# Kernel optimization log

Hardware: AMD Instinct MI355X
Metric: run time of the kernel (lower is better)

The kernel has to match this reference:

```python
import jax, jax.numpy as jnp
import numpy as np

NEG_INF = -1e9


def setup_inputs() -> dict:
    key = jax.random.key(0)
    ks = jax.random.split(key, 8)
    B, S, D = 8, 2048, 1024
    scale = 1.0 / np.sqrt(D)
    src = jax.random.normal(ks[0], (B, S, D), dtype=jnp.float32)
    pad_len = jax.random.randint(ks[1], (B,), 0, S // 10)
    pos = jnp.arange(S)[None, :]
    src_padding_mask = jnp.where(pos >= (S - pad_len)[:, None], NEG_INF, 0.0).astype(jnp.float32)[:, :, None]
    # causal (subsequent) additive mask [S,S]
    src_subsq_mask = jnp.where(jnp.triu(jnp.ones((S, S), dtype=bool), k=1), NEG_INF, 0.0).astype(jnp.float32)
    Wk = jax.random.normal(ks[2], (D, D), dtype=jnp.float32) * scale
    Wv = jax.random.normal(ks[3], (D, D), dtype=jnp.float32) * scale
    Wq = jax.random.normal(ks[4], (D, D), dtype=jnp.float32) * scale
    bk = jnp.zeros((D,), dtype=jnp.float32)
    bv = jnp.zeros((D,), dtype=jnp.float32)
    bq = jnp.zeros((D,), dtype=jnp.float32)
    return {"src": src, "src_padding_mask": src_padding_mask, "src_subsq_mask": src_subsq_mask,
            "Wk": Wk, "bk": bk, "Wv": Wv, "bv": bv, "Wq": Wq, "bq": bq}


def reference(src, src_padding_mask, src_subsq_mask, Wk, bk, Wv, bv, Wq, bq):
    d_model = src.shape[-1]
    # torch nn.Linear: x @ W.T + b
    keys = jnp.einsum('bsd,ed->bse', src, Wk) + bk
    values = jnp.einsum('bsd,ed->bse', src, Wv) + bv
    queries = jnp.einsum('bsd,ed->bse', src, Wq) + bq
    sqrt_d = jnp.asarray(d_model, src.dtype) ** 0.5
    att = jnp.einsum('bqd,bkd->bqk', queries, keys) / sqrt_d   # [B,S,S]
    att = att + jnp.swapaxes(src_padding_mask, 1, 2)           # [B,1,S] broadcast
    att = att + src_subsq_mask[None, :, :]                      # [1,S,S] broadcast
    att_softmax = jax.nn.softmax(att, axis=2)
    att_out = jnp.einsum('bqk,bkd->bqd', att_softmax, values)
    return att_out
```

## Files before the change

### kernel.cpp

```cpp
#include <hip/hip_runtime.h>
#include <cstdint>
#include <cstddef>

#define BATCH 8
#define SEQ   2048
#define DM    1024

typedef _Float16 half8 __attribute__((ext_vector_type(8)));
typedef _Float16 half4v __attribute__((ext_vector_type(4)));
typedef float floatx4 __attribute__((ext_vector_type(4)));
typedef float float4v __attribute__((ext_vector_type(4)));

#define GLOBAL_AS __attribute__((address_space(1)))
#define LDS_AS    __attribute__((address_space(3)))

__device__ __forceinline__ void gl_lds16(const _Float16* g, _Float16* l) {
    __builtin_amdgcn_global_load_lds((const GLOBAL_AS void*)g, (LDS_AS void*)l, 16, 0, 0);
}

__device__ __forceinline__ void stage128(const _Float16* __restrict__ g, int ld, int k0,
                                         _Float16* l, int wave, int lane) {
    const int rw = wave * 8 + (lane >> 3);
    const int sl = lane & 7;
    #pragma unroll
    for (int i = 0; i < 2; i++) {
        const int r = i * 64 + rw;
        gl_lds16(g + (size_t)r * ld + k0 + ((sl ^ (r & 7)) << 3),
                 l + ((i * 64 + wave * 8) << 6));
    }
}

#define SCHED __builtin_amdgcn_sched_barrier(0)
#define BAR   __builtin_amdgcn_s_barrier()
#define WAIT_VM0    asm volatile("s_waitcnt vmcnt(0)" ::: "memory")
#define WAIT_LGKM12 asm volatile("s_waitcnt lgkmcnt(12)" ::: "memory")
#define WAIT_LGKM0  asm volatile("s_waitcnt lgkmcnt(0)" ::: "memory")

#define RD_SET(AV, BV, BUF, SL)                                               \
    _Pragma("unroll")                                                         \
    for (int i_ = 0; i_ < 4; i_++)                                            \
        AV[i_] = *(const half8*)&SA[BUF][aoff + i_ * 1024 + (SL)];            \
    _Pragma("unroll")                                                         \
    for (int i_ = 0; i_ < 4; i_++)                                            \
        AV[4 + i_] = *(const half8*)&SA[BUF][aoff + 8192 + i_ * 1024 + (SL)]; \
    _Pragma("unroll")                                                         \
    for (int j_ = 0; j_ < 2; j_++)                                            \
        BV[j_] = *(const half8*)&SB[BUF][boff + j_ * 4096 + (SL)];            \
    _Pragma("unroll")                                                         \
    for (int j_ = 0; j_ < 2; j_++)                                            \
        BV[2 + j_] = *(const half8*)&SB[BUF][boff + 8192 + j_ * 4096 + (SL)];

#define MM_SET(AV, BV)                                                        \
    __builtin_amdgcn_s_setprio(1);                                            \
    _Pragma("unroll")                                                         \
    for (int i_ = 0; i_ < 8; i_++)                                            \
        _Pragma("unroll")                                                     \
        for (int j_ = 0; j_ < 4; j_++)                                        \
            acc[i_][j_] = __builtin_amdgcn_mfma_f32_16x16x32_f16(             \
                AV[i_], BV[j_], acc[i_][j_], 0, 0, 0);                        \
    __builtin_amdgcn_s_setprio(0);

__device__ __forceinline__ void gemm256_rr(
    const _Float16* __restrict__ A, const _Float16* __restrict__ B,
    int lda, int ldb, int nkt,
    _Float16 (&SA)[2][16384], _Float16 (&SB)[2][16384],
    floatx4 (&acc)[8][4])
{
    const int t = threadIdx.x;
    const int wave = t >> 6, lane = t & 63;
    const int l15 = lane & 15, kq = lane >> 4;
    const int wm = wave >> 2, wn = wave & 3;

    const int aoff = (wm * 64 + l15) << 6;
    const int boff = (wn * 16 + l15) << 6;
    const int sl0 = ((kq ^ (l15 & 7)) << 3);
    const int sl1 = (((4 + kq) ^ (l15 & 7)) << 3);

    const _Float16* A128 = A + (size_t)128 * lda;
    const _Float16* B128 = B + (size_t)128 * ldb;

    half8 a0[8], b0[4], a1[8], b1[4];

    stage128(A,    lda, 0, &SA[0][0],    wave, lane);
    stage128(A128, lda, 0, &SA[0][8192], wave, lane);
    stage128(B,    ldb, 0, &SB[0][0],    wave, lane);
    stage128(B128, ldb, 0, &SB[0][8192], wave, lane);
    WAIT_VM0; BAR; SCHED;
    RD_SET(a0, b0, 0, sl0);

    for (int kt = 0; kt < nkt; ++kt) {
        const int bs = kt & 1;
        const bool more = (kt + 1) < nkt;
        if (more) {
            const int k1 = (kt + 1) * 64;
            stage128(A,    lda, k1, &SA[bs ^ 1][0],    wave, lane);
            stage128(A128, lda, k1, &SA[bs ^ 1][8192], wave, lane);
            stage128(B,    ldb, k1, &SB[bs ^ 1][0],    wave, lane);
            stage128(B128, ldb, k1, &SB[bs ^ 1][8192], wave, lane);
        }
        RD_SET(a1, b1, bs, sl1);
        WAIT_LGKM12; SCHED;
        MM_SET(a0, b0);
        WAIT_LGKM0; SCHED;
        if (more) {
            WAIT_VM0;
            BAR; SCHED;
            RD_SET(a0, b0, bs ^ 1, sl0);
        }
        MM_SET(a1, b1);
    }
}

__global__ __launch_bounds__(256) void convert_inputs(
    const float* __restrict__ src,
    const float* __restrict__ Wk, const float* __restrict__ Wv, const float* __restrict__ Wq,
    _Float16* __restrict__ Xh, _Float16* __restrict__ Wh)
{
    const int gid = blockIdx.x * 256 + threadIdx.x;
    const int gs  = gridDim.x * 256;
    const int nX4 = BATCH * SEQ * DM / 4;
    const int nW4 = DM * DM / 4;
    const float4v* s4  = (const float4v*)src;
    const float4v* wk4 = (const float4v*)Wk;
    const float4v* wv4 = (const float4v*)Wv;
    const float4v* wq4 = (const float4v*)Wq;
    half4v* x4 = (half4v*)Xh;
    half4v* w4 = (half4v*)Wh;
    for (int i = gid; i < nX4; i += gs) {
        float4v v = s4[i];
        half4v h;
        #pragma unroll
        for (int e = 0; e < 4; e++) h[e] = (_Float16)v[e];
        x4[i] = h;
    }
    for (int i = gid; i < nW4; i += gs) {
        float4v a = wk4[i], b = wv4[i], c = wq4[i];
        half4v ha, hb, hc;
        #pragma unroll
        for (int e = 0; e < 4; e++) { ha[e] = (_Float16)a[e]; hb[e] = (_Float16)b[e]; hc[e] = (_Float16)c[e]; }
        w4[i]           = ha;
        w4[nW4 + i]     = hb;
        w4[2 * nW4 + i] = hc;
    }
}

__global__ __launch_bounds__(512, 2) void qkv_gemm(
    const _Float16* __restrict__ Xh, const _Float16* __restrict__ Wh,
    const float* __restrict__ bk, const float* __restrict__ bv, const float* __restrict__ bq,
    _Float16* __restrict__ Kh, _Float16* __restrict__ Vt, _Float16* __restrict__ Qh)
{
    __shared__ __align__(16) _Float16 SA[2][16384];
    __shared__ __align__(16) _Float16 SB[2][16384];
    const int L = blockIdx.x;
    const int lid = (L & 7) * 96 + (L >> 3);
    const int z = lid >> 8;
    const int r = lid & 255;
    int by, bx;
    const _Float16 *A, *B;
    if (z == 1) {
        by = r & 3; bx = r >> 2;
        A = Wh + (size_t)DM * DM + (size_t)by * 256 * DM;
        B = Xh + (size_t)bx * 256 * DM;
    } else {
        by = r >> 2; bx = r & 3;
        A = Xh + (size_t)by * 256 * DM;
        B = Wh + (z ? (size_t)2 * DM * DM : (size_t)0) + (size_t)bx * 256 * DM;
    }
    floatx4 acc[8][4] = {};
    gemm256_rr(A, B, DM, DM, 16, SA, SB, acc);

    const int t = threadIdx.x, wave = t >> 6, lane = t & 63;
    const int l15 = lane & 15, kq = lane >> 4;
    const int wm = wave >> 2, wn = wave & 3;
    if (z == 1) {
        #pragma unroll
        for (int i = 0; i < 8; i++)
            #pragma unroll
            for (int j = 0; j < 4; j++)
                #pragma unroll
                for (int rr = 0; rr < 4; rr++) {
                    const int d  = by * 256 + wm * 64 + (i & 3) * 16 + (i >> 2) * 128 + kq * 4 + rr;
                    const int sg = bx * 256 + wn * 16 + (j & 1) * 64 + (j >> 1) * 128 + l15;
                    const int b = sg >> 11, s = sg & (SEQ - 1);
                    Vt[((size_t)b * DM + d) * SEQ + s] = (_Float16)(acc[i][j][rr] + bv[d]);
                }
    } else {
        const float* bias = z ? bq : bk;
        _Float16* outp    = z ? Qh : Kh;
        #pragma unroll
        for (int i = 0; i < 8; i++)
            #pragma unroll
            for (int j = 0; j < 4; j++)
                #pragma unroll
                for (int rr = 0; rr < 4; rr++) {
                    const int row = by * 256 + wm * 64 + (i & 3) * 16 + (i >> 2) * 128 + kq * 4 + rr;
                    const int col = bx * 256 + wn * 16 + (j & 1) * 64 + (j >> 1) * 128 + l15;
                    outp[(size_t)row * DM + col] = (_Float16)(acc[i][j][rr] + bias[col]);
                }
    }
}

__global__ __launch_bounds__(512, 2) void scores_gemm(
    const _Float16* __restrict__ Qh, const _Float16* __restrict__ Kh,
    const float* __restrict__ pad, _Float16* __restrict__ Sc)
{
    __shared__ __align__(16) _Float16 SA[2][16384];
    __shared__ __align__(16) _Float16 SB[2][16384];
    const int L = blockIdx.x;
    const int lid = (L & 7) * 36 + (L >> 3);
    const int b = lid / 36, tri = lid - b * 36;
    int by = 0;
    #pragma unroll
    for (int u = 1; u <= 7; u++) if (tri >= (u * (u + 1)) / 2) by = u;
    const int bx = tri - (by * (by + 1)) / 2;

    const _Float16* A = Qh + ((size_t)b * SEQ + by * 256) * DM;
    const _Float16* B = Kh + ((size_t)b * SEQ + bx * 256) * DM;
    floatx4 acc[8][4] = {};
    gemm256_rr(A, B, DM, DM, 16, SA, SB, acc);

    const int t = threadIdx.x, wave = t >> 6, lane = t & 63;
    const int l15 = lane & 15, kq = lane >> 4;
    const int wm = wave >> 2, wn = wave & 3;
    #pragma unroll
    for (int i = 0; i < 8; i++)
        #pragma unroll
        for (int j = 0; j < 4; j++)
            #pragma unroll
            for (int rr = 0; rr < 4; rr++) {
                const int row = by * 256 + wm * 64 + (i & 3) * 16 + (i >> 2) * 128 + kq * 4 + rr;
                const int col = bx * 256 + wn * 16 + (j & 1) * 64 + (j >> 1) * 128 + l15;
                Sc[((size_t)b * SEQ + row) * SEQ + col] =
                    (_Float16)(acc[i][j][rr] * 0.03125f + pad[b * SEQ + col]);
            }
}

__global__ __launch_bounds__(256) void softmax_rows(_Float16* __restrict__ Sc)
{
    const int bid = blockIdx.x;
    const int b = bid >> 11, q = bid & (SEQ - 1);
    _Float16* row = Sc + ((size_t)b * SEQ + q) * SEQ;
    const int n = q + 1;
    const int kmaxr = ((q >> 8) + 1) << 8;
    const int t = threadIdx.x;
    const int c0 = t * 8;
    const bool active = (c0 < kmaxr);
    __shared__ float red[4];

    half8 v = {};
    if (active) v = *(const half8*)(row + c0);
    float f[8];
    float m = -3.0e38f;
    #pragma unroll
    for (int e = 0; e < 8; e++) {
        f[e] = (active && (c0 + e < n)) ? (float)v[e] : -3.0e38f;
        m = fmaxf(m, f[e]);
    }
    #pragma unroll
    for (int o = 32; o > 0; o >>= 1) m = fmaxf(m, __shfl_down(m, o));
    if ((t & 63) == 0) red[t >> 6] = m;
    __syncthreads();
    m = fmaxf(fmaxf(red[0], red[1]), fmaxf(red[2], red[3]));

    float ex[8], s = 0.f;
    #pragma unroll
    for (int e = 0; e < 8; e++) {
        ex[e] = (f[e] > -1.0e38f) ? __expf(f[e] - m) : 0.f;
        s += ex[e];
    }
    #pragma unroll
    for (int o = 32; o > 0; o >>= 1) s += __shfl_down(s, o);
    __syncthreads();
    if ((t & 63) == 0) red[t >> 6] = s;
    __syncthreads();
    s = red[0] + red[1] + red[2] + red[3];

    if (active) {
        const float inv = 1.0f / s;
        half8 o8;
        #pragma unroll
        for (int e = 0; e < 8; e++) o8[e] = (_Float16)(ex[e] * inv);
        *(half8*)(row + c0) = o8;
    }
}

__global__ __launch_bounds__(512, 2) void pv_gemm(
    const _Float16* __restrict__ P, const _Float16* __restrict__ Vt,
    float* __restrict__ out)
{
    __shared__ __align__(16) _Float16 SA[2][16384];
    __shared__ __align__(16) _Float16 SB[2][16384];
    const int L = blockIdx.x;
    const int lid = (L & 7) * 32 + (L >> 3);
    const int b = lid >> 5, r = lid & 31;
    const int by = 7 - (r >> 2);
    const int bx = r & 3;

    const _Float16* A = P  + ((size_t)b * SEQ + by * 256) * SEQ;
    const _Float16* B = Vt + ((size_t)b * DM  + bx * 256) * SEQ;
    const int nkt = (by + 1) * 4;
    floatx4 acc[8][4] = {};
    gemm256_rr(A, B, SEQ, SEQ, nkt, SA, SB, acc);

    const int t = threadIdx.x, wave = t >> 6, lane = t & 63;
    const int l15 = lane & 15, kq = lane >> 4;
    const int wm = wave >> 2, wn = wave & 3;
    #pragma unroll
    for (int i = 0; i < 8; i++)
        #pragma unroll
        for (int j = 0; j < 4; j++)
            #pragma unroll
            for (int rr = 0; rr < 4; rr++) {
                const int row = by * 256 + wm * 64 + (i & 3) * 16 + (i >> 2) * 128 + kq * 4 + rr;
                const int col = bx * 256 + wn * 16 + (j & 1) * 64 + (j >> 1) * 128 + l15;
                out[((size_t)b * SEQ + row) * DM + col] = acc[i][j][rr];
            }
}

extern "C" void kernel_launch(void* const* d_in, const int* in_sizes, int n_in,
                              void* d_out, int out_size, void* d_ws, size_t ws_size,
                              hipStream_t stream) {
    const float* src = (const float*)d_in[0];
    const float* pad = (const float*)d_in[1];
    const float* Wk = (const float*)d_in[3];
    const float* bk = (const float*)d_in[4];
    const float* Wv = (const float*)d_in[5];
    const float* bv = (const float*)d_in[6];
    const float* Wq = (const float*)d_in[7];
    const float* bq = (const float*)d_in[8];
    float* out = (float*)d_out;

    char* ws = (char*)d_ws;
    _Float16* Wh = (_Float16*)(ws);
    _Float16* Qh = (_Float16*)(ws + 6291456);
    _Float16* Kh = (_Float16*)(ws + 39845888);
    _Float16* Vt = (_Float16*)(ws + 73400320);
    _Float16* Sc = (_Float16*)(ws + 106954752);
    _Float16* Xh = (_Float16*)d_out;

    convert_inputs<<<2048, 256, 0, stream>>>(src, Wk, Wv, Wq, Xh, Wh);
    qkv_gemm<<<768, 512, 0, stream>>>(Xh, Wh, bk, bv, bq, Kh, Vt, Qh);
    scores_gemm<<<288, 512, 0, stream>>>(Qh, Kh, pad, Sc);
    softmax_rows<<<BATCH * SEQ, 256, 0, stream>>>(Sc);
    pv_gemm<<<256, 512, 0, stream>>>(Sc, Vt, out);
}
```

Baseline: 382.9 us.

## Interleave global-to-LDS staging and LDS reads with MFMA groups in GEMM loop

Measured after the change: 384.2 us. Within noise of the previous version (+0.3%).

```diff
diff --git a/kernel.cpp b/kernel.cpp
--- a/kernel.cpp
+++ b/kernel.cpp
@@ -34,28 +34,33 @@
 #define BAR   __builtin_amdgcn_s_barrier()
 #define WAIT_VM0    asm volatile("s_waitcnt vmcnt(0)" ::: "memory")
 #define WAIT_LGKM12 asm volatile("s_waitcnt lgkmcnt(12)" ::: "memory")
+#define WAIT_LGKM6  asm volatile("s_waitcnt lgkmcnt(6)" ::: "memory")
+#define WAIT_LGKM4  asm volatile("s_waitcnt lgkmcnt(4)" ::: "memory")
 #define WAIT_LGKM0  asm volatile("s_waitcnt lgkmcnt(0)" ::: "memory")
 
-#define RD_SET(AV, BV, BUF, SL)                                               \
+#define RD_A03(AV, BUF, SL)                                                   \
     _Pragma("unroll")                                                         \
     for (int i_ = 0; i_ < 4; i_++)                                            \
-        AV[i_] = *(const half8*)&SA[BUF][aoff + i_ * 1024 + (SL)];            \
+        AV[i_] = *(const half8*)&SA[BUF][aoff + i_ * 1024 + (SL)];
+#define RD_A47(AV, BUF, SL)                                                   \
     _Pragma("unroll")                                                         \
     for (int i_ = 0; i_ < 4; i_++)                                            \
-        AV[4 + i_] = *(const half8*)&SA[BUF][aoff + 8192 + i_ * 1024 + (SL)]; \
+        AV[4 + i_] = *(const half8*)&SA[BUF][aoff + 8192 + i_ * 1024 + (SL)];
+#define RD_B01(BV, BUF, SL)                                                   \
     _Pragma("unroll")                                                         \
     for (int j_ = 0; j_ < 2; j_++)                                            \
-        BV[j_] = *(const half8*)&SB[BUF][boff + j_ * 4096 + (SL)];            \
+        BV[j_] = *(const half8*)&SB[BUF][boff + j_ * 4096 + (SL)];
+#define RD_B23(BV, BUF, SL)                                                   \
     _Pragma("unroll")                                                         \
     for (int j_ = 0; j_ < 2; j_++)                                            \
         BV[2 + j_] = *(const half8*)&SB[BUF][boff + 8192 + j_ * 4096 + (SL)];
 
-#define MM_SET(AV, BV)                                                        \
+#define MM_G(AV, BV, I0, IN, J0, JN)                                          \
     __builtin_amdgcn_s_setprio(1);                                            \
     _Pragma("unroll")                                                         \
-    for (int i_ = 0; i_ < 8; i_++)                                            \
+    for (int i_ = (I0); i_ < (I0) + (IN); i_++)                               \
         _Pragma("unroll")                                                     \
-        for (int j_ = 0; j_ < 4; j_++)                                        \
+        for (int j_ = (J0); j_ < (J0) + (JN); j_++)                           \
             acc[i_][j_] = __builtin_amdgcn_mfma_f32_16x16x32_f16(             \
                 AV[i_], BV[j_], acc[i_][j_], 0, 0, 0);                        \
     __builtin_amdgcn_s_setprio(0);
@@ -86,28 +91,39 @@
     stage128(B,    ldb, 0, &SB[0][0],    wave, lane);
     stage128(B128, ldb, 0, &SB[0][8192], wave, lane);
     WAIT_VM0; BAR; SCHED;
-    RD_SET(a0, b0, 0, sl0);
+    RD_A03(a0, 0, sl0); RD_B01(b0, 0, sl0);
+    RD_B23(b0, 0, sl0); RD_A47(a0, 0, sl0);
 
     for (int kt = 0; kt < nkt; ++kt) {
         const int bs = kt & 1;
         const bool more = (kt + 1) < nkt;
-        if (more) {
-            const int k1 = (kt + 1) * 64;
-            stage128(A,    lda, k1, &SA[bs ^ 1][0],    wave, lane);
-            stage128(A128, lda, k1, &SA[bs ^ 1][8192], wave, lane);
-            stage128(B,    ldb, k1, &SB[bs ^ 1][0],    wave, lane);
-            stage128(B128, ldb, k1, &SB[bs ^ 1][8192], wave, lane);
-        }
-        RD_SET(a1, b1, bs, sl1);
+        const int k1 = (kt + 1) * 64;
+
+        if (more) stage128(A, lda, k1, &SA[bs ^ 1][0], wave, lane);
+        RD_A03(a1, bs, sl1); RD_B01(b1, bs, sl1);
         WAIT_LGKM12; SCHED;
-        MM_SET(a0, b0);
+        MM_G(a0, b0, 0, 4, 0, 2);
+        if (more) stage128(A128, lda, k1, &SA[bs ^ 1][8192], wave, lane);
+        RD_B23(b1, bs, sl1);
+        WAIT_LGKM12; SCHED;
+        MM_G(a0, b0, 0, 4, 2, 2);
+        if (more) stage128(B, ldb, k1, &SB[bs ^ 1][0], wave, lane);
+        RD_A47(a1, bs, sl1);
+        WAIT_LGKM12; SCHED;
+        MM_G(a0, b0, 4, 4, 0, 4);
+        if (more) stage128(B128, ldb, k1, &SB[bs ^ 1][8192], wave, lane);
+        WAIT_LGKM6; SCHED;
+        MM_G(a1, b1, 0, 4, 0, 2);
+        WAIT_LGKM4; SCHED;
+        MM_G(a1, b1, 0, 4, 2, 2);
         WAIT_LGKM0; SCHED;
         if (more) {
             WAIT_VM0;
             BAR; SCHED;
-            RD_SET(a0, b0, bs ^ 1, sl0);
+            RD_A03(a0, bs ^ 1, sl0); RD_B01(b0, bs ^ 1, sl0);
+            RD_B23(b0, bs ^ 1, sl0); RD_A47(a0, bs ^ 1, sl0);
         }
-        MM_SET(a1, b1);
+        MM_G(a1, b1, 4, 4, 0, 4);
     }
 }
 
```

## Replace double-buffered K=64 QKV GEMM loop with 4-stage K=32 pipeline

Applied to the files above, without the earlier changes.

After: 411.3 us. +7.4%, slower.

```diff
diff --git a/kernel.cpp b/kernel.cpp
--- a/kernel.cpp
+++ b/kernel.cpp
@@ -18,6 +18,78 @@
     __builtin_amdgcn_global_load_lds((const GLOBAL_AS void*)g, (LDS_AS void*)l, 16, 0, 0);
 }
 
+#define SCHED __builtin_amdgcn_sched_barrier(0)
+#define BAR   __builtin_amdgcn_s_barrier()
+#define WAIT_VM0    asm volatile("s_waitcnt vmcnt(0)" ::: "memory")
+#define WAIT_VM8    asm volatile("s_waitcnt vmcnt(8)" ::: "memory")
+#define WAIT_VM4    asm volatile("s_waitcnt vmcnt(4)" ::: "memory")
+#define WAIT_LGKM12 asm volatile("s_waitcnt lgkmcnt(12)" ::: "memory")
+#define WAIT_LGKM0  asm volatile("s_waitcnt lgkmcnt(0)" ::: "memory")
+
+__device__ __forceinline__ void stage32(const _Float16* __restrict__ g, int ld, int k0,
+                                        _Float16* l, int wave, int lane) {
+    const int chunk = ((lane & 3) ^ ((lane >> 3) & 3)) << 3;
+    #pragma unroll
+    for (int i = 0; i < 2; i++) {
+        const int row = i * 128 + wave * 16 + (lane >> 2);
+        gl_lds16(g + (size_t)row * ld + k0 + chunk,
+                 l + i * 4096 + wave * 512);
+    }
+}
+
+__device__ __forceinline__ void gemm256_p4(
+    const _Float16* __restrict__ A, const _Float16* __restrict__ B,
+    int lda, int ldb, int nkt,
+    _Float16 (&SA)[4][8192], _Float16 (&SB)[4][8192],
+    floatx4 (&acc)[8][4])
+{
+    const int t = threadIdx.x;
+    const int wave = t >> 6, lane = t & 63;
+    const int l15 = lane & 15, kq = lane >> 4;
+    const int wm = wave >> 2, wn = wave & 3;
+    const int sl = ((kq ^ ((l15 >> 1) & 3)) << 3);
+    const int aoff = (wm * 64 + l15) * 32 + sl;
+    const int boff = (wn * 16 + l15) * 32 + sl;
+
+    half8 a[8], b[4];
+
+    stage32(A, lda, 0,  &SA[0][0], wave, lane);
+    stage32(B, ldb, 0,  &SB[0][0], wave, lane);
+    stage32(A, lda, 32, &SA[1][0], wave, lane);
+    stage32(B, ldb, 32, &SB[1][0], wave, lane);
+    stage32(A, lda, 64, &SA[2][0], wave, lane);
+    stage32(B, ldb, 64, &SB[2][0], wave, lane);
+    WAIT_VM8;
+    BAR;
+
+    for (int kt = 0; kt < nkt; ++kt) {
+        const int m = kt & 3;
+        if (kt + 3 < nkt) {
+            const int k3 = (kt + 3) * 32, m3 = (kt + 3) & 3;
+            stage32(A, lda, k3, &SA[m3][0], wave, lane);
+            stage32(B, ldb, k3, &SB[m3][0], wave, lane);
+        }
+        #pragma unroll
+        for (int i = 0; i < 8; i++)
+            a[i] = *(const half8*)&SA[m][aoff + (i & 3) * 512 + (i >> 2) * 4096];
+        #pragma unroll
+        for (int j = 0; j < 4; j++)
+            b[j] = *(const half8*)&SB[m][boff + (j & 1) * 2048 + (j >> 1) * 4096];
+        __builtin_amdgcn_s_setprio(1);
+        #pragma unroll
+        for (int i = 0; i < 8; i++)
+            #pragma unroll
+            for (int j = 0; j < 4; j++)
+                acc[i][j] = __builtin_amdgcn_mfma_f32_16x16x32_f16(
+                    a[i], b[j], acc[i][j], 0, 0, 0);
+        __builtin_amdgcn_s_setprio(0);
+        WAIT_LGKM0;
+        if (kt + 3 < nkt)      { WAIT_VM8; BAR; }
+        else if (kt + 2 < nkt) { WAIT_VM4; BAR; }
+        else if (kt + 1 < nkt) { WAIT_VM0; BAR; }
+    }
+}
+
 __device__ __forceinline__ void stage128(const _Float16* __restrict__ g, int ld, int k0,
                                          _Float16* l, int wave, int lane) {
     const int rw = wave * 8 + (lane >> 3);
@@ -30,13 +102,7 @@
     }
 }
 
-#define SCHED __builtin_amdgcn_sched_barrier(0)
-#define BAR   __builtin_amdgcn_s_barrier()
-#define WAIT_VM0    asm volatile("s_waitcnt vmcnt(0)" ::: "memory")
-#define WAIT_LGKM12 asm volatile("s_waitcnt lgkmcnt(12)" ::: "memory")
-#define WAIT_LGKM0  asm volatile("s_waitcnt lgkmcnt(0)" ::: "memory")
-
-#define RD_SET(AV, BV, BUF, SL)                                               \
+#define RD_SETR(AV, BV, BUF, SL)                                              \
     _Pragma("unroll")                                                         \
     for (int i_ = 0; i_ < 4; i_++)                                            \
         AV[i_] = *(const half8*)&SA[BUF][aoff + i_ * 1024 + (SL)];            \
@@ -50,7 +116,7 @@
     for (int j_ = 0; j_ < 2; j_++)                                            \
         BV[2 + j_] = *(const half8*)&SB[BUF][boff + 8192 + j_ * 4096 + (SL)];
 
-#define MM_SET(AV, BV)                                                        \
+#define MM_SETR(AV, BV)                                                       \
     __builtin_amdgcn_s_setprio(1);                                            \
     _Pragma("unroll")                                                         \
     for (int i_ = 0; i_ < 8; i_++)                                            \
@@ -86,7 +152,7 @@
     stage128(B,    ldb, 0, &SB[0][0],    wave, lane);
     stage128(B128, ldb, 0, &SB[0][8192], wave, lane);
     WAIT_VM0; BAR; SCHED;
-    RD_SET(a0, b0, 0, sl0);
+    RD_SETR(a0, b0, 0, sl0);
 
     for (int kt = 0; kt < nkt; ++kt) {
         const int bs = kt & 1;
@@ -98,16 +164,16 @@
             stage128(B,    ldb, k1, &SB[bs ^ 1][0],    wave, lane);
             stage128(B128, ldb, k1, &SB[bs ^ 1][8192], wave, lane);
         }
-        RD_SET(a1, b1, bs, sl1);
+        RD_SETR(a1, b1, bs, sl1);
         WAIT_LGKM12; SCHED;
-        MM_SET(a0, b0);
+        MM_SETR(a0, b0);
         WAIT_LGKM0; SCHED;
         if (more) {
             WAIT_VM0;
             BAR; SCHED;
-            RD_SET(a0, b0, bs ^ 1, sl0);
+            RD_SETR(a0, b0, bs ^ 1, sl0);
         }
-        MM_SET(a1, b1);
+        MM_SETR(a1, b1);
     }
 }
 
@@ -149,8 +215,8 @@
     const float* __restrict__ bk, const float* __restrict__ bv, const float* __restrict__ bq,
     _Float16* __restrict__ Kh, _Float16* __restrict__ Vt, _Float16* __restrict__ Qh)
 {
-    __shared__ __align__(16) _Float16 SA[2][16384];
-    __shared__ __align__(16) _Float16 SB[2][16384];
+    __shared__ __align__(16) _Float16 SA[4][8192];
+    __shared__ __align__(16) _Float16 SB[4][8192];
     const int L = blockIdx.x;
     const int lid = (L & 7) * 96 + (L >> 3);
     const int z = lid >> 8;
@@ -167,7 +233,7 @@
         B = Wh + (z ? (size_t)2 * DM * DM : (size_t)0) + (size_t)bx * 256 * DM;
     }
     floatx4 acc[8][4] = {};
-    gemm256_rr(A, B, DM, DM, 16, SA, SB, acc);
+    gemm256_p4(A, B, DM, DM, 32, SA, SB, acc);
 
     const int t = threadIdx.x, wave = t >> 6, lane = t & 63;
     const int l15 = lane & 15, kq = lane >> 4;
```
